# Kernel optimization log

Hardware: AMD Instinct MI355X
Metric: run time of the kernel (lower is better)

Reference implementation:

```python
import jax, jax.numpy as jnp
import numpy as np

EMBED_DIM = 1024
N_TOKENS = 8192


def setup_inputs() -> dict:
    key = jax.random.key(0)
    k1, k2, k3 = jax.random.split(key, 3)
    inputs = jax.random.normal(k1, (N_TOKENS, EMBED_DIM), dtype=jnp.float32)
    rotation_params = jax.random.normal(k2, (EMBED_DIM, EMBED_DIM), dtype=jnp.float32)
    entangle_params = jax.random.normal(k3, (EMBED_DIM, EMBED_DIM), dtype=jnp.float32)
    return {"inputs": inputs, "rotation_params": rotation_params, "entangle_params": entangle_params}


def reference(inputs, rotation_params, entangle_params):
    # query/key projections from externally supplied params
    embed_dim = inputs.shape[-1]
    wq = rotation_params.reshape(embed_dim, -1)
    wk = entangle_params.reshape(embed_dim, -1)
    query = inputs @ wq          # [N, d]
    key = inputs @ wk            # [N, d]
    scale = 1.0 / jnp.sqrt(jnp.float32(embed_dim))
    scores = jax.nn.softmax(jnp.einsum('nd,md->nm', query, key) * scale, axis=-1)  # [N, N]
    context = scores @ inputs    # attend over raw inputs (V = inputs)
    return context
```

## Files before the change

kernel.cpp:

```cpp
#include <hip/hip_runtime.h>
#include <hip/hip_bf16.h>


typedef _Float16 f16x8 __attribute__((ext_vector_type(8)));
typedef float    f32x4 __attribute__((ext_vector_type(4)));

__device__ __forceinline__ void g2lds16(const _Float16* g, _Float16* l) {
    __builtin_amdgcn_global_load_lds(
        (__attribute__((address_space(1))) unsigned int*)(g),
        (__attribute__((address_space(3))) unsigned int*)(l),
        16, 0, 0);
}


__global__ void prep_x(const float* __restrict__ src,
                       _Float16* __restrict__ hi, _Float16* __restrict__ lo,
                       _Float16* __restrict__ xt, int R, int C) {
    __shared__ float tile[32][33];
    int c0 = blockIdx.x * 32, r0 = blockIdx.y * 32;
    int tx = threadIdx.x, ty = threadIdx.y;
#pragma unroll
    for (int k = 0; k < 4; ++k) {
        int r = ty + 8 * k;
        size_t idx = (size_t)(r0 + r) * C + c0 + tx;
        float v = src[idx];
        tile[r][tx] = v;
        _Float16 h = (_Float16)v;
        hi[idx] = h;
        lo[idx] = (_Float16)(v - (float)h);
    }
    __syncthreads();
#pragma unroll
    for (int k = 0; k < 4; ++k) {
        float v = tile[tx][ty + 8 * k];
        xt[(size_t)(c0 + ty + 8 * k) * R + r0 + tx] = (_Float16)v;
    }
}

__global__ void transpose_split(const float* __restrict__ src,
                                _Float16* __restrict__ dhi,
                                _Float16* __restrict__ dlo,
                                int R, int C) {
    __shared__ float tile[32][33];
    int c0 = blockIdx.x * 32, r0 = blockIdx.y * 32;
    int tx = threadIdx.x, ty = threadIdx.y;
#pragma unroll
    for (int k = 0; k < 4; ++k)
        tile[ty + 8 * k][tx] = src[(size_t)(r0 + ty + 8 * k) * C + c0 + tx];
    __syncthreads();
#pragma unroll
    for (int k = 0; k < 4; ++k) {
        float v = tile[tx][ty + 8 * k];
        _Float16 h = (_Float16)v;
        size_t idx = (size_t)(c0 + ty + 8 * k) * R + r0 + tx;
        dhi[idx] = h;
        dlo[idx] = (_Float16)(v - (float)h);
    }
}

__global__ __launch_bounds__(256) void add_rows(const float* __restrict__ a,
                                                const float* __restrict__ b,
                                                float* __restrict__ out, long n4) {
    long i = (long)blockIdx.x * blockDim.x + threadIdx.x;
    long stride = (long)gridDim.x * blockDim.x;
    for (; i < n4; i += stride) {
        float4 x = ((const float4*)a)[i];
        float4 y = ((const float4*)b)[i];
        x.x += y.x; x.y += y.y; x.z += y.z; x.w += y.w;
        ((float4*)out)[i] = x;
    }
}

template <int TERMS, int BKH, int SWAP, int SPLIT_OUT>
__global__ __launch_bounds__(512, 2) void gemm_p4(
    const _Float16* __restrict__ Ahi, const _Float16* __restrict__ Alo,
    const _Float16* __restrict__ Bhi, const _Float16* __restrict__ Blo,
    float* __restrict__ C, _Float16* __restrict__ Chi, _Float16* __restrict__ Clo,
    long lda, long ldb, long ldc, int K, int nrb, int ncb,
    long zA, long zB, long zC) {
    static_assert(BKH == 32 || BKH == 64, "");
    constexpr int NMAT = (TERMS == 3) ? 4 : 2;
    constexpr int KK   = BKH / 32;
    constexpr int LPR  = BKH / 8;
    constexpr int MATH = 256 * BKH;
    __shared__ __align__(16) _Float16 s[2][NMAT * MATH];

    const long z = blockIdx.z;
    Ahi += z * zA; Bhi += z * zB;
    if constexpr (TERMS == 3) { Alo += z * zA; Blo += z * zB; }
    if constexpr (SPLIT_OUT) { Chi += z * zC; Clo += z * zC; }
    else C += z * zC;

    const int nb = nrb * ncb;
    const int orig = blockIdx.x;
    const int q = nb >> 3, r8 = nb & 7;
    const int xcd = orig & 7, pos = orig >> 3;
    const int sw = (xcd < r8 ? xcd * (q + 1) : r8 * (q + 1) + (xcd - r8) * q) + pos;
    int rb, cb;
    if constexpr (SWAP) { rb = sw / ncb; cb = sw % ncb; }
    else                { cb = sw / nrb; rb = sw % nrb; }
    const long rowBase = (long)rb * 256;
    const long colBase = (long)cb * 256;

    const int t = threadIdx.x;
    const int wave = t >> 6;
    const int lane = t & 63;
    const int lm = lane & 15;
    const int lq = lane >> 4;
    const int wr = wave >> 2;
    const int wc = wave & 3;
    const int wg = wave & 3;

    const int ri   = lane / LPR;
    const int slot = lane % LPR;
    const int swzW = (BKH == 32) ? ((ri >> 1) & 3) : (ri & 7);
    const int colOff = (slot ^ swzW) * 8;

    const _Float16* gB[4]; int lB[4];
    const _Float16* gA[4]; int lA[4];
#pragma unroll
    for (int b = 0; b < 4; ++b) {
        if constexpr (TERMS == 3) {
            const int rowW = (b >> 1) * 128 + wave * 16;
            const _Float16* m = (b & 1) ? Blo : Bhi;
            gB[b] = m + (colBase + rowW + ri) * ldb + colOff;
            lB[b] = (2 + (b & 1)) * MATH + rowW * BKH;
        } else {
            const int rowW = b * 64 + wave * 8;
            gB[b] = Bhi + (colBase + rowW + ri) * ldb + colOff;
            lB[b] = MATH + rowW * BKH;
        }
    }
#pragma unroll
    for (int a = 0; a < 4; ++a) {
        if constexpr (TERMS == 3) {
            const int rowW = wr * 128 + (a >> 1) * 64 + wg * 16;
            const _Float16* m = (a & 1) ? Alo : Ahi;
            gA[a] = m + (rowBase + rowW + ri) * lda + colOff;
            lA[a] = (a & 1) * MATH + rowW * BKH;
        } else {
            const int rowW = wr * 128 + a * 32 + wg * 8;
            gA[a] = Ahi + (rowBase + rowW + ri) * lda + colOff;
            lA[a] = rowW * BKH;
        }
    }

    const int swzR = (BKH == 32) ? ((lm >> 1) & 3) : (lm & 7);

    f32x4 acc[8][4];
#pragma unroll
    for (int rr = 0; rr < 8; ++rr)
#pragma unroll
        for (int cc = 0; cc < 4; ++cc)
#pragma unroll
            for (int i = 0; i < 4; ++i) acc[rr][cc][i] = 0.0f;

    const int NT = K / BKH;

#define VMW(N) asm volatile("s_waitcnt vmcnt(" #N ")" ::: "memory")
#define STB(b, buf, k0) g2lds16(gB[b] + (k0), &s[buf][lB[b]])
#define STA(a, buf, k0) g2lds16(gA[a] + (k0), &s[buf][lA[a]])

    STB(0, 0, 0); STB(1, 0, 0); STB(2, 0, 0); STB(3, 0, 0);
    STA(0, 0, 0); STA(1, 0, 0); STA(2, 0, 0); STA(3, 0, 0);
    if constexpr (TERMS == 3) { VMW(2); } else { VMW(3); }
    __builtin_amdgcn_s_barrier();

    int cur = 0;
    for (int tt = 0; tt < NT; ++tt) {
        const int nxt = cur ^ 1;
        const bool nl = (tt + 1 < NT);
        const long k1 = (long)(tt + 1) * BKH;
        const _Float16* sAh = &s[cur][0];
        const _Float16* sAl = sAh + MATH;
        const _Float16* sBh = sAh + (TERMS == 3 ? 2 : 1) * MATH;
        const _Float16* sBl = sAh + 3 * MATH;
        f16x8 bh[4 * KK], bl[TERMS == 3 ? 4 * KK : 1];
#pragma unroll
        for (int p = 0; p < 4; ++p) {
            f16x8 ah[2 * KK], al[TERMS == 3 ? 2 * KK : 1];
#pragma unroll
            for (int rr = 0; rr < 2; ++rr) {
                const int arow = wr * 128 + (2 * p + rr) * 16 + lm;
#pragma unroll
                for (int kk = 0; kk < KK; ++kk) {
                    const int off = arow * BKH + (((kk * 4 + lq) ^ swzR) << 3);
                    ah[rr * KK + kk] = *(const f16x8*)&sAh[off];
                    if constexpr (TERMS == 3)
                        al[rr * KK + kk] = *(const f16x8*)&sAl[off];
                }
            }
            if (p == 0) {
#pragma unroll
                for (int cc = 0; cc < 4; ++cc) {
                    const int brow = wc * 64 + cc * 16 + lm;
#pragma unroll
                    for (int kk = 0; kk < KK; ++kk) {
                        const int off = brow * BKH + (((kk * 4 + lq) ^ swzR) << 3);
                        bh[cc * KK + kk] = *(const f16x8*)&sBh[off];
                        if constexpr (TERMS == 3)
                            bl[cc * KK + kk] = *(const f16x8*)&sBl[off];
                    }
                }
            }
            if (nl) {
                if (p == 0)      { STB(0, nxt, k1); STB(1, nxt, k1);
                                   STB(2, nxt, k1); STB(3, nxt, k1); }
                else if (p == 1) { STA(0, nxt, k1); STA(1, nxt, k1); }
                else if (p == 2) { STA(2, nxt, k1); }
                else             { STA(3, nxt, k1); }
            }
            if constexpr (TERMS == 3) {
                if (p == 1)      { if (nl) { VMW(5); } else { VMW(0); } }
                else if (p == 3) { if (nl) { VMW(2); } }
            } else {
                if (p == 0)      { if (nl) { VMW(6); } else { VMW(2); } }
                else if (p == 1) { if (nl) { VMW(6); } else { VMW(1); } }
                else if (p == 2) { if (nl) { VMW(7); } else { VMW(0); } }
                else             { if (nl) { VMW(3); } }
            }
            __builtin_amdgcn_s_barrier();
            asm volatile("s_waitcnt lgkmcnt(0)" ::: "memory");
            __builtin_amdgcn_sched_barrier(0);
            __builtin_amdgcn_s_setprio(1);
#pragma unroll
            for (int rr = 0; rr < 2; ++rr)
#pragma unroll
                for (int cc = 0; cc < 4; ++cc)
#pragma unroll
                    for (int kk = 0; kk < KK; ++kk) {
                        acc[2 * p + rr][cc] = __builtin_amdgcn_mfma_f32_16x16x32_f16(
                            ah[rr * KK + kk], bh[cc * KK + kk], acc[2 * p + rr][cc], 0, 0, 0);
                        if constexpr (TERMS == 3) {
                            acc[2 * p + rr][cc] = __builtin_amdgcn_mfma_f32_16x16x32_f16(
                                ah[rr * KK + kk], bl[cc * KK + kk], acc[2 * p + rr][cc], 0, 0, 0);
                            acc[2 * p + rr][cc] = __builtin_amdgcn_mfma_f32_16x16x32_f16(
                                al[rr * KK + kk], bh[cc * KK + kk], acc[2 * p + rr][cc], 0, 0, 0);
                        }
                    }
            __builtin_amdgcn_s_setprio(0);
            __builtin_amdgcn_s_barrier();
        }
        cur = nxt;
    }
#undef VMW
#undef STB
#undef STA

#pragma unroll
    for (int rr = 0; rr < 8; ++rr)
#pragma unroll
        for (int cc = 0; cc < 4; ++cc)
#pragma unroll
            for (int i = 0; i < 4; ++i) {
                const long row = rowBase + wr * 128 + rr * 16 + lq * 4 + i;
                const long col = colBase + wc * 64 + cc * 16 + lm;
                if constexpr (SPLIT_OUT) {
                    float v = acc[rr][cc][i];
                    _Float16 h = (_Float16)v;
                    Chi[row * ldc + col] = h;
                    Clo[row * ldc + col] = (_Float16)(v - (float)h);
                } else {
                    C[row * ldc + col] = acc[rr][cc][i];
                }
            }
}

__global__ __launch_bounds__(256) void softmax_rows(const float* __restrict__ S,
                                                    _Float16* __restrict__ P,
                                                    long ldp, int N) {
    const int row = blockIdx.x;
    const int t = threadIdx.x;
    const float4* rowp = (const float4*)(S + (size_t)row * N);
    float4 v[8];
    float mx = -3.4e38f;
#pragma unroll
    for (int g = 0; g < 4; ++g) {
        v[2 * g]     = rowp[2 * t + 512 * g];
        v[2 * g + 1] = rowp[2 * t + 512 * g + 1];
    }
#pragma unroll
    for (int i = 0; i < 8; ++i)
        mx = fmaxf(mx, fmaxf(fmaxf(v[i].x, v[i].y), fmaxf(v[i].z, v[i].w)));
    __shared__ float red[8];
#pragma unroll
    for (int off = 32; off >= 1; off >>= 1) mx = fmaxf(mx, __shfl_xor(mx, off));
    if ((t & 63) == 0) red[t >> 6] = mx;
    __syncthreads();
    mx = fmaxf(fmaxf(red[0], red[1]), fmaxf(red[2], red[3]));

    float sum = 0.0f;
#pragma unroll
    for (int i = 0; i < 8; ++i) {
        v[i].x = __expf((v[i].x - mx) * 0.03125f);
        v[i].y = __expf((v[i].y - mx) * 0.03125f);
        v[i].z = __expf((v[i].z - mx) * 0.03125f);
        v[i].w = __expf((v[i].w - mx) * 0.03125f);
        sum += (v[i].x + v[i].y) + (v[i].z + v[i].w);
    }
#pragma unroll
    for (int off = 32; off >= 1; off >>= 1) sum += __shfl_xor(sum, off);
    if ((t & 63) == 0) red[4 + (t >> 6)] = sum;
    __syncthreads();
    float inv = 1.0f / (red[4] + red[5] + red[6] + red[7]);

    f16x8* prow = (f16x8*)(P + (size_t)row * ldp);
#pragma unroll
    for (int g = 0; g < 4; ++g) {
        float4 a = v[2 * g], b = v[2 * g + 1];
        f16x8 o;
        o[0] = (_Float16)(a.x * inv); o[1] = (_Float16)(a.y * inv);
        o[2] = (_Float16)(a.z * inv); o[3] = (_Float16)(a.w * inv);
        o[4] = (_Float16)(b.x * inv); o[5] = (_Float16)(b.y * inv);
        o[6] = (_Float16)(b.z * inv); o[7] = (_Float16)(b.w * inv);
        prow[t + 256 * g] = o;
    }
}

extern "C" void kernel_launch(void* const* d_in, const int* in_sizes, int n_in,
                              void* d_out, int out_size, void* d_ws, size_t ws_size,
                              hipStream_t stream) {
    const float* X  = (const float*)d_in[0];
    const float* Wq = (const float*)d_in[1];
    const float* Wk = (const float*)d_in[2];
    float* out = (float*)d_out;

    const long Nt = 8192, D = 1024;
    char* ws = (char*)d_ws;
    const size_t MB = 1024ull * 1024ull;

    _Float16* XT  = (_Float16*)(ws + 0);
    _Float16* Qhi = (_Float16*)(ws + 16 * MB);
    _Float16* Qlo = (_Float16*)(ws + 32 * MB);
    _Float16* Khi = (_Float16*)(ws + 48 * MB);
    _Float16* Klo = (_Float16*)(ws + 64 * MB);
    _Float16* Xhi   = (_Float16*)(ws + 80 * MB);
    _Float16* Xlo   = (_Float16*)(ws + 96 * MB);
    _Float16* WqThi = (_Float16*)(ws + 112 * MB);
    _Float16* WqTlo = (_Float16*)(ws + 114 * MB);
    _Float16* WkThi = (_Float16*)(ws + 116 * MB);
    _Float16* WkTlo = (_Float16*)(ws + 118 * MB);
    float* PK0 = (float*)(ws + 16 * MB);

    const size_t rowBytes = (size_t)Nt * 4;
    const bool planA = ws_size >= 208 * MB + 256 * rowBytes;
    _Float16* Pbuf = (_Float16*)(ws + 80 * MB);
    float* Sc;
    long chunk;
    if (planA) {
        Sc = (float*)(ws + 208 * MB);
        size_t avail = ws_size - 208 * MB;
        chunk = (long)((avail / rowBytes / 256) * 256);
    } else {
        Sc = (float*)(ws + 80 * MB);
        size_t avail = ws_size > 80 * MB ? ws_size - 80 * MB : 0;
        chunk = (long)((avail / rowBytes / 256) * 256);
        if (chunk < 256) chunk = 256;
    }
    if (chunk > Nt) chunk = Nt;
    {
        long nch = (Nt + chunk - 1) / chunk;
        chunk = (((Nt + nch - 1) / nch) + 255) / 256 * 256;
    }

    prep_x<<<dim3(32, 256), dim3(32, 8), 0, stream>>>(X, Xhi, Xlo, XT,
                                                      (int)Nt, (int)D);
    transpose_split<<<dim3(32, 32), dim3(32, 8), 0, stream>>>(Wq, WqThi, WqTlo,
                                                              (int)D, (int)D);
    transpose_split<<<dim3(32, 32), dim3(32, 8), 0, stream>>>(Wk, WkThi, WkTlo,
                                                              (int)D, (int)D);

    gemm_p4<3, 32, 1, 1><<<dim3(32 * 4, 1, 2), 512, 0, stream>>>(
        Xhi, Xlo, WqThi, WqTlo, nullptr, Qhi, Qlo,
        D, D, D, (int)D, 32, 4,
        0, (long)(4 * MB / 2), (long)(32 * MB / 2));

    long done = 0;
    while (done < Nt) {
        long cur = Nt - done < chunk ? Nt - done : chunk;
        int nrb = (int)(cur / 256), ncb = (int)(Nt / 256);
        gemm_p4<3, 32, 1, 0><<<dim3(nrb * ncb, 1, 1), 512, 0, stream>>>(
            Qhi + done * D, Qlo + done * D, Khi, Klo, Sc, nullptr, nullptr,
            D, D, Nt, (int)D, nrb, ncb, 0, 0, 0);
        if (planA) {
            softmax_rows<<<(int)cur, 256, 0, stream>>>(Sc, Pbuf + done * Nt,
                                                       Nt, (int)Nt);
        } else {
            softmax_rows<<<(int)cur, 256, 0, stream>>>(Sc, (_Float16*)Sc,
                                                       2 * Nt, (int)Nt);
            gemm_p4<1, 64, 1, 0><<<dim3((int)(cur / 256) * 4, 1, 1), 512, 0, stream>>>(
                (const _Float16*)Sc, nullptr, XT, nullptr,
                out + done * D, nullptr, nullptr,
                2 * Nt, Nt, D, (int)Nt, (int)(cur / 256), 4, 0, 0, 0);
        }
        done += cur;
    }

    if (planA) {
        gemm_p4<1, 64, 1, 0><<<dim3(32 * 4, 1, 2), 512, 0, stream>>>(
            Pbuf, nullptr, XT, nullptr, PK0, nullptr, nullptr,
            Nt, Nt, D, (int)(Nt / 2), 32, 4,
            Nt / 2, Nt / 2, Nt * D);
        add_rows<<<1024, 256, 0, stream>>>(PK0, PK0 + Nt * D, out, Nt * D / 4);
    }
}
```

Before: 822.0 us.

## Split P@V GEMM 8-way over K per chunk, store fp16 partials in score buffer

Drops the planA path that materialised the whole P matrix. Each score chunk now runs its P@X GEMM as an 8-way split-K, so a small chunk still launches enough blocks to fill the GPU. The fp16 partial sums go into the unused upper half of each score row, and a new add_gran kernel reduces the eight partials into the fp32 output. This trades extra partial traffic and an fp16 rounding of the partial sums for more parallelism and less workspace. It also runs one extra reduction kernel per chunk.

```diff
diff --git a/kernel.cpp b/kernel.cpp
--- a/kernel.cpp
+++ b/kernel.cpp
@@ -58,20 +58,24 @@
     }
 }
 
-__global__ __launch_bounds__(256) void add_rows(const float* __restrict__ a,
-                                                const float* __restrict__ b,
-                                                float* __restrict__ out, long n4) {
-    long i = (long)blockIdx.x * blockDim.x + threadIdx.x;
-    long stride = (long)gridDim.x * blockDim.x;
-    for (; i < n4; i += stride) {
-        float4 x = ((const float4*)a)[i];
-        float4 y = ((const float4*)b)[i];
-        x.x += y.x; x.y += y.y; x.z += y.z; x.w += y.w;
-        ((float4*)out)[i] = x;
-    }
-}
-
-template <int TERMS, int BKH, int SWAP, int SPLIT_OUT>
+__global__ __launch_bounds__(128) void add_gran(const _Float16* __restrict__ g,
+                                                float* __restrict__ out) {
+    const long r = blockIdx.x;
+    const int t = threadIdx.x;
+    const _Float16* base = g + r * 16384 + 8192 + t * 8;
+    float acc[8] = {0, 0, 0, 0, 0, 0, 0, 0};
+#pragma unroll
+    for (int z = 0; z < 8; ++z) {
+        f16x8 v = *(const f16x8*)(base + z * 1024);
+#pragma unroll
+        for (int i = 0; i < 8; ++i) acc[i] += (float)v[i];
+    }
+    float4* o = (float4*)(out + r * 1024 + t * 8);
+    o[0] = make_float4(acc[0], acc[1], acc[2], acc[3]);
+    o[1] = make_float4(acc[4], acc[5], acc[6], acc[7]);
+}
+
+template <int TERMS, int BKH, int SWAP, int SPLIT_OUT, int GRAN>
 __global__ __launch_bounds__(512, 2) void gemm_p4(
     const _Float16* __restrict__ Ahi, const _Float16* __restrict__ Alo,
     const _Float16* __restrict__ Bhi, const _Float16* __restrict__ Blo,
@@ -89,7 +93,7 @@
     Ahi += z * zA; Bhi += z * zB;
     if constexpr (TERMS == 3) { Alo += z * zA; Blo += z * zB; }
     if constexpr (SPLIT_OUT) { Chi += z * zC; Clo += z * zC; }
-    else C += z * zC;
+    else if constexpr (!GRAN) C += z * zC;
 
     const int nb = nrb * ncb;
     const int orig = blockIdx.x;
@@ -255,7 +259,10 @@
             for (int i = 0; i < 4; ++i) {
                 const long row = rowBase + wr * 128 + rr * 16 + lq * 4 + i;
                 const long col = colBase + wc * 64 + cc * 16 + lm;
-                if constexpr (SPLIT_OUT) {
+                if constexpr (GRAN) {
+                    Chi[row * 16384 + 8192 + z * 1024 + col] =
+                        (_Float16)acc[rr][cc][i];
+                } else if constexpr (SPLIT_OUT) {
                     float v = acc[rr][cc][i];
                     _Float16 h = (_Float16)v;
                     Chi[row * ldc + col] = h;
@@ -340,23 +347,12 @@
     _Float16* WqTlo = (_Float16*)(ws + 114 * MB);
     _Float16* WkThi = (_Float16*)(ws + 116 * MB);
     _Float16* WkTlo = (_Float16*)(ws + 118 * MB);
-    float* PK0 = (float*)(ws + 16 * MB);
 
     const size_t rowBytes = (size_t)Nt * 4;
-    const bool planA = ws_size >= 208 * MB + 256 * rowBytes;
-    _Float16* Pbuf = (_Float16*)(ws + 80 * MB);
-    float* Sc;
-    long chunk;
-    if (planA) {
-        Sc = (float*)(ws + 208 * MB);
-        size_t avail = ws_size - 208 * MB;
-        chunk = (long)((avail / rowBytes / 256) * 256);
-    } else {
-        Sc = (float*)(ws + 80 * MB);
-        size_t avail = ws_size > 80 * MB ? ws_size - 80 * MB : 0;
-        chunk = (long)((avail / rowBytes / 256) * 256);
-        if (chunk < 256) chunk = 256;
-    }
+    float* Sc = (float*)(ws + 80 * MB);
+    size_t avail = ws_size > 80 * MB ? ws_size - 80 * MB : 0;
+    long chunk = (long)((avail / rowBytes / 256) * 256);
+    if (chunk < 256) chunk = 256;
     if (chunk > Nt) chunk = Nt;
     {
         long nch = (Nt + chunk - 1) / chunk;
@@ -370,7 +366,7 @@
     transpose_split<<<dim3(32, 32), dim3(32, 8), 0, stream>>>(Wk, WkThi, WkTlo,
                                                               (int)D, (int)D);
 
-    gemm_p4<3, 32, 1, 1><<<dim3(32 * 4, 1, 2), 512, 0, stream>>>(
+    gemm_p4<3, 32, 1, 1, 0><<<dim3(32 * 4, 1, 2), 512, 0, stream>>>(
         Xhi, Xlo, WqThi, WqTlo, nullptr, Qhi, Qlo,
         D, D, D, (int)D, 32, 4,
         0, (long)(4 * MB / 2), (long)(32 * MB / 2));
@@ -379,28 +375,18 @@
     while (done < Nt) {
         long cur = Nt - done < chunk ? Nt - done : chunk;
         int nrb = (int)(cur / 256), ncb = (int)(Nt / 256);
-        gemm_p4<3, 32, 1, 0><<<dim3(nrb * ncb, 1, 1), 512, 0, stream>>>(
+        gemm_p4<3, 32, 1, 0, 0><<<dim3(nrb * ncb, 1, 1), 512, 0, stream>>>(
             Qhi + done * D, Qlo + done * D, Khi, Klo, Sc, nullptr, nullptr,
             D, D, Nt, (int)D, nrb, ncb, 0, 0, 0);
-        if (planA) {
-            softmax_rows<<<(int)cur, 256, 0, stream>>>(Sc, Pbuf + done * Nt,
-                                                       Nt, (int)Nt);
-        } else {
-            softmax_rows<<<(int)cur, 256, 0, stream>>>(Sc, (_Float16*)Sc,
-                                                       2 * Nt, (int)Nt);
-            gemm_p4<1, 64, 1, 0><<<dim3((int)(cur / 256) * 4, 1, 1), 512, 0, stream>>>(
-                (const _Float16*)Sc, nullptr, XT, nullptr,
-                out + done * D, nullptr, nullptr,
-                2 * Nt, Nt, D, (int)Nt, (int)(cur / 256), 4, 0, 0, 0);
-        }
+        softmax_rows<<<(int)cur, 256, 0, stream>>>(Sc, (_Float16*)Sc,
+                                                   2 * Nt, (int)Nt);
+        gemm_p4<1, 64, 1, 0, 1><<<dim3(nrb * 4, 1, 8), 512, 0, stream>>>(
+            (const _Float16*)Sc, nullptr, XT, nullptr,
+            nullptr, (_Float16*)Sc, nullptr,
+            2 * Nt, Nt, D, (int)(Nt / 8), nrb, 4,
+            Nt / 8, Nt / 8, 0);
+        add_gran<<<(int)cur, 128, 0, stream>>>((const _Float16*)Sc,
+                                               out + done * D);
         done += cur;
     }
-
-    if (planA) {
-        gemm_p4<1, 64, 1, 0><<<dim3(32 * 4, 1, 2), 512, 0, stream>>>(
-            Pbuf, nullptr, XT, nullptr, PK0, nullptr, nullptr,
-            Nt, Nt, D, (int)(Nt / 2), 32, 4,
-            Nt / 2, Nt / 2, Nt * D);
-        add_rows<<<1024, 256, 0, stream>>>(PK0, PK0 + Nt * D, out, Nt * D / 4);
-    }
-}
+}
```

Measured after the change: 741.7 us. 9.8% less time.
